# Performance work log

Measured on AMD Instinct MI355X. Metric: run time of the kernel, lower is better.

Reference implementation:

```python
import jax, jax.numpy as jnp
import numpy as np

BATCH, SEQ = 2, 4096
IN_FEATURES = 4096
OUT_FEATURES = 4096
BLOCK = 64                      # oft_block_size (bs)
RANK = IN_FEATURES // BLOCK     # number of diagonal blocks (r)


def setup_inputs() -> dict:
    key = jax.random.key(0)
    k1, k2, k3, k4 = jax.random.split(key, 4)
    x = jax.random.normal(k1, (BATCH, SEQ, IN_FEATURES), dtype=jnp.float32)
    # OFT adapter parameters: one (bs x bs) generator per block
    oft_r = jax.random.normal(k2, (RANK, BLOCK, BLOCK), dtype=jnp.float32) * 0.02
    # Dequantized GPTQ weight (out_features x in_features) + bias
    W = jax.random.normal(k3, (OUT_FEATURES, IN_FEATURES), dtype=jnp.float32) * 0.02
    b = jax.random.normal(k4, (OUT_FEATURES,), dtype=jnp.float32)
    return {"x": x, "oft_r": oft_r, "W": W, "b": b}


def _cayley_batch(data):
    # data: [r, bs, bs].  Q = (I - skew) @ (I + skew)^{-1}  (torch.linalg.solve left=False)
    bs = data.shape[-1]
    skew = 0.5 * (data - jnp.swapaxes(data, -1, -2))
    I = jnp.eye(bs, dtype=data.dtype)
    A = I + skew   # [r, bs, bs]
    B = I - skew
    # Solve Q A = B  ->  A^T Q^T = B^T
    Qt = jnp.linalg.solve(jnp.swapaxes(A, -1, -2), jnp.swapaxes(B, -1, -2))
    return jnp.swapaxes(Qt, -1, -2)


def reference(x, oft_r, W, b):
    rank, bs, _ = oft_r.shape
    # oft_rotation starts as identity; single active adapter -> rotation = Cayley(oft_r)
    oft_rotation = _cayley_batch(oft_r)            # [rank, bs, bs]
    batch_dims = x.shape[:-1]
    x_reshaped = x.reshape(*batch_dims, rank, bs)  # [..., r, k]
    x_rot = jnp.einsum('...rk,rkc->...rc', x_reshaped, oft_rotation)
    x_rot = x_rot.reshape(*batch_dims, rank * bs)  # [..., in_features]
    # quant_linear_module (dequantized): y = x_rot @ W^T + b
    return jnp.einsum('bsi,oi->bso', x_rot, W) + b
```

## Files before the change

### kernel.cpp

```cpp
#include <hip/hip_runtime.h>
#include <hip/hip_bf16.h>
#include <stdint.h>


typedef __bf16 bf16;
typedef __attribute__((ext_vector_type(4))) __bf16 bf16x4;
typedef __attribute__((ext_vector_type(8))) __bf16 bf16x8;
typedef __attribute__((ext_vector_type(4))) float f32x4;

__device__ __forceinline__ bf16 f2bf(float f) {
  unsigned u = __builtin_bit_cast(unsigned, f);
  u += 0x7fffu + ((u >> 16) & 1u);
  unsigned short h = (unsigned short)(u >> 16);
  return __builtin_bit_cast(bf16, h);
}

__global__ __launch_bounds__(256) void prep_kernel(const float* __restrict__ oft_r,
                                                   float* __restrict__ Qxt,
                                                   const float* __restrict__ x,
                                                   bf16* __restrict__ xb, long n) {
  __shared__ float St[64][68];
  __shared__ float Ta[64][65];
  __shared__ float Tb[64][65];
  const int tid = threadIdx.x;

  if (blockIdx.x >= 64) {
    long i0 = ((long)(blockIdx.x - 64) * 256 + tid) * 8;
    long stride = (long)(gridDim.x - 64) * 256 * 8;
    for (long i = i0; i < n; i += stride) {
      f32x4 a = *reinterpret_cast<const f32x4*>(x + i);
      f32x4 b = *reinterpret_cast<const f32x4*>(x + i + 4);
      bf16x8 o;
      o[0] = f2bf(a[0]); o[1] = f2bf(a[1]); o[2] = f2bf(a[2]); o[3] = f2bf(a[3]);
      o[4] = f2bf(b[0]); o[5] = f2bf(b[1]); o[6] = f2bf(b[2]); o[7] = f2bf(b[3]);
      *reinterpret_cast<bf16x8*>(xb + i) = o;
    }
    return;
  }

  const int r = blockIdx.x;
  const float* D = oft_r + (size_t)r * 4096;

  for (int idx = tid; idx < 4096; idx += 256) {
    int i = idx >> 6, j = idx & 63;
    float s = 0.5f * (D[i * 64 + j] - D[j * 64 + i]);
    St[j][i] = s;
    Ta[i][j] = (i == j ? 1.0f : 0.0f) - s;
  }
  __syncthreads();

  const int j = tid & 63;
  const int w = tid >> 6;
  float (*Tin)[65] = Ta;
  float (*Tout)[65] = Tb;

  for (int it = 0; it < 5; ++it) {
    float out[16];
#pragma unroll
    for (int m = 0; m < 16; ++m) out[m] = ((w * 16 + m) == j ? 1.0f : 0.0f);
    for (int c = 0; c < 64; ++c) {
      float tc = Tin[c][j];
      f32x4 s0 = *reinterpret_cast<const f32x4*>(&St[c][w * 16]);
      f32x4 s1 = *reinterpret_cast<const f32x4*>(&St[c][w * 16 + 4]);
      f32x4 s2 = *reinterpret_cast<const f32x4*>(&St[c][w * 16 + 8]);
      f32x4 s3 = *reinterpret_cast<const f32x4*>(&St[c][w * 16 + 12]);
#pragma unroll
      for (int q = 0; q < 4; ++q) {
        out[q]      -= s0[q] * tc;
        out[4 + q]  -= s1[q] * tc;
        out[8 + q]  -= s2[q] * tc;
        out[12 + q] -= s3[q] * tc;
      }
    }
#pragma unroll
    for (int m = 0; m < 16; ++m) Tout[w * 16 + m][j] = out[m];
    __syncthreads();
    float (*tmp)[65] = Tin; Tin = Tout; Tout = tmp;
  }
  {
    float out[16];
#pragma unroll
    for (int m = 0; m < 16; ++m) out[m] = Tin[w * 16 + m][j];
    for (int c = 0; c < 64; ++c) {
      float tc = Tin[c][j];
      f32x4 s0 = *reinterpret_cast<const f32x4*>(&St[c][w * 16]);
      f32x4 s1 = *reinterpret_cast<const f32x4*>(&St[c][w * 16 + 4]);
      f32x4 s2 = *reinterpret_cast<const f32x4*>(&St[c][w * 16 + 8]);
      f32x4 s3 = *reinterpret_cast<const f32x4*>(&St[c][w * 16 + 12]);
#pragma unroll
      for (int q = 0; q < 4; ++q) {
        out[q]      -= s0[q] * tc;
        out[4 + q]  -= s1[q] * tc;
        out[8 + q]  -= s2[q] * tc;
        out[12 + q] -= s3[q] * tc;
      }
    }
#pragma unroll
    for (int m = 0; m < 16; ++m) Qxt[(size_t)r * 4096 + (w * 16 + m) * 64 + j] = out[m];
  }
}

__global__ __launch_bounds__(256) void fold_w_kernel(const float* __restrict__ W,
                                                     const float* __restrict__ Qxt,
                                                     bf16* __restrict__ Wp) {
  __shared__ bf16 Wb[128 * 64];
  __shared__ bf16 Xt[64 * 64];
  const int tid = threadIdx.x;
  const int lane = tid & 63;
  const int wave = tid >> 6;
  const int o0 = blockIdx.x * 128;
  const int r = blockIdx.y;
  const int fr = lane & 15;
  const int kg = lane >> 4;

#pragma unroll
  for (int i = 0; i < 8; ++i) {
    int c = i * 256 + tid;
    int row = c >> 4, c4 = c & 15;
    f32x4 v = *reinterpret_cast<const f32x4*>(W + (size_t)(o0 + row) * 4096 + r * 64 + c4 * 4);
    bf16x4 o; o[0] = f2bf(v[0]); o[1] = f2bf(v[1]); o[2] = f2bf(v[2]); o[3] = f2bf(v[3]);
    *reinterpret_cast<bf16x4*>(&Wb[row * 64 + c4 * 4]) = o;
  }
#pragma unroll
  for (int i = 0; i < 4; ++i) {
    int c = i * 256 + tid;
    int row = c >> 4, c4 = c & 15;
    f32x4 v = *reinterpret_cast<const f32x4*>(Qxt + (size_t)r * 4096 + row * 64 + c4 * 4);
    bf16x4 o; o[0] = f2bf(v[0]); o[1] = f2bf(v[1]); o[2] = f2bf(v[2]); o[3] = f2bf(v[3]);
    *reinterpret_cast<bf16x4*>(&Xt[row * 64 + c4 * 4]) = o;
  }
  __syncthreads();

  const int wm = wave * 32;
  f32x4 acc[2][4];
#pragma unroll
  for (int mi = 0; mi < 2; ++mi)
#pragma unroll
    for (int ni = 0; ni < 4; ++ni) acc[mi][ni] = (f32x4){0.f, 0.f, 0.f, 0.f};

#pragma unroll
  for (int kk = 0; kk < 64; kk += 32) {
    bf16x8 af[2], bx[4];
#pragma unroll
    for (int mi = 0; mi < 2; ++mi)
      af[mi] = *reinterpret_cast<const bf16x8*>(&Wb[(wm + mi * 16 + fr) * 64 + kk + kg * 8]);
#pragma unroll
    for (int ni = 0; ni < 4; ++ni)
      bx[ni] = *reinterpret_cast<const bf16x8*>(&Xt[(ni * 16 + fr) * 64 + kk + kg * 8]);
#pragma unroll
    for (int mi = 0; mi < 2; ++mi)
#pragma unroll
      for (int ni = 0; ni < 4; ++ni)
        acc[mi][ni] = __builtin_amdgcn_mfma_f32_16x16x32_bf16(af[mi], bx[ni], acc[mi][ni], 0, 0, 0);
  }

#pragma unroll
  for (int mi = 0; mi < 2; ++mi)
#pragma unroll
    for (int ni = 0; ni < 4; ++ni)
#pragma unroll
      for (int q = 0; q < 4; ++q) {
        int row = o0 + wm + mi * 16 + kg * 4 + q;
        int col = ni * 16 + fr;
        Wp[(size_t)row * 4096 + r * 64 + col] = f2bf(acc[mi][ni][q]);
      }
}


#define GLDS16(g, l) __builtin_amdgcn_global_load_lds( \
    (const __attribute__((address_space(1))) unsigned int*)(g), \
    (__attribute__((address_space(3))) unsigned int*)(l), 16, 0, 0)

#define VMCNT4 asm volatile("s_waitcnt vmcnt(4)" ::: "memory")
#define VMCNT0 asm volatile("s_waitcnt vmcnt(0)" ::: "memory")
#define BARRIER() do { asm volatile("" ::: "memory"); \
  __builtin_amdgcn_s_barrier(); asm volatile("" ::: "memory"); } while (0)

#define MFMA16(AF, BF, RB) \
  _Pragma("unroll") \
  for (int m_ = 0; m_ < 4; ++m_) \
    _Pragma("unroll") \
    for (int n_ = 0; n_ < 4; ++n_) \
      acc[RB + m_][n_] = __builtin_amdgcn_mfma_f32_16x16x32_bf16(AF[m_], BF[n_], acc[RB + m_][n_], 0, 0, 0);

#define DO_TILE(BUF, TN, PRE) do { \
     \
    _Pragma("unroll") for (int n_ = 0; n_ < 4; ++n_) Ob[n_] = LDB(BUF, 0, n_); \
    _Pragma("unroll") for (int m_ = 0; m_ < 4; ++m_) Oa[m_] = LDA(BUF, 0, m_); \
    if (PRE) STAGE(TN, BUF ^ 1, 0); \
    BARRIER(); \
    __builtin_amdgcn_s_setprio(1); MFMA16(Oa, Ob, 0) __builtin_amdgcn_s_setprio(0); \
    BARRIER(); \
     \
    _Pragma("unroll") for (int m_ = 0; m_ < 4; ++m_) Ea[m_] = LDA(BUF, 0, 4 + m_); \
    if (PRE) STAGE(TN, BUF ^ 1, 1); \
    if (PRE) { VMCNT4; } else { VMCNT0; } \
    BARRIER(); \
    __builtin_amdgcn_s_setprio(1); MFMA16(Ea, Ob, 4) __builtin_amdgcn_s_setprio(0); \
    BARRIER(); \
     \
    _Pragma("unroll") for (int n_ = 0; n_ < 4; ++n_) Eb[n_] = LDB(BUF, 1, n_); \
    _Pragma("unroll") for (int m_ = 0; m_ < 4; ++m_) Oa[m_] = LDA(BUF, 1, m_); \
    if (PRE) STAGE(TN, BUF ^ 1, 2); \
    BARRIER(); \
    __builtin_amdgcn_s_setprio(1); MFMA16(Oa, Eb, 0) __builtin_amdgcn_s_setprio(0); \
    BARRIER(); \
     \
    _Pragma("unroll") for (int m_ = 0; m_ < 4; ++m_) Ea[m_] = LDA(BUF, 1, 4 + m_); \
    if (PRE) STAGE(TN, BUF ^ 1, 3); \
    if (PRE) { VMCNT4; } else { VMCNT0; } \
    BARRIER(); \
    __builtin_amdgcn_s_setprio(1); MFMA16(Ea, Eb, 4) __builtin_amdgcn_s_setprio(0); \
    BARRIER(); \
  } while (0)

__global__ __launch_bounds__(512, 2) void gemm_kernel(const bf16* __restrict__ A,
                                                      const bf16* __restrict__ B,
                                                      const float* __restrict__ bias,
                                                      float* __restrict__ C,
                                                      int M, int N, int K) {
  __shared__ bf16 lds[65536];
  const int tid = threadIdx.x;
  const int lane = tid & 63;
  const int wave = tid >> 6;
  const int wr = wave >> 2;
  const int wc = wave & 3;
  const int fr = lane & 15;
  const int kg = lane >> 4;
  const int m0 = blockIdx.y * 256;
  const int n0 = blockIdx.x * 256;
  const int NT = K >> 6;

  f32x4 acc[8][4];
#pragma unroll
  for (int m = 0; m < 8; ++m)
#pragma unroll
    for (int n = 0; n < 4; ++n) acc[m][n] = (f32x4){0.f, 0.f, 0.f, 0.f};

  auto STAGE = [&](int t, int db, int p) {
    const int op = p & 1, ks = p >> 1;
    const bf16* src = op ? B : A;
    const int base_row = op ? n0 : m0;
    const int ldsb = db * 32768 + op * 16384 + ks * 8192;
#pragma unroll
    for (int i = 0; i < 2; ++i) {
      int c = i * 512 + tid;
      int row = c >> 2, cc = c & 3;
      const bf16* g = src + (size_t)(base_row + row) * K + t * 64 + ks * 32
                      + ((cc ^ ((row >> 1) & 3)) << 3);
      GLDS16(g, &lds[ldsb + ((i * 512 + wave * 64) << 3)]);
    }
  };
  auto LDA = [&](int buf, int ks, int mi) -> bf16x8 {
    int row = wr * 128 + mi * 16 + fr;
    return *reinterpret_cast<const bf16x8*>(
        &lds[buf * 32768 + ks * 8192 + row * 32 + ((kg ^ ((row >> 1) & 3)) << 3)]);
  };
  auto LDB = [&](int buf, int ks, int ni) -> bf16x8 {
    int row = wc * 64 + ni * 16 + fr;
    return *reinterpret_cast<const bf16x8*>(
        &lds[buf * 32768 + 16384 + ks * 8192 + row * 32 + ((kg ^ ((row >> 1) & 3)) << 3)]);
  };

#pragma unroll
  for (int p = 0; p < 4; ++p) STAGE(0, 0, p);
  VMCNT4;
  BARRIER();

  bf16x8 Oa[4], Ob[4], Ea[4], Eb[4];
  for (int t = 0; t < NT; t += 2) {
    DO_TILE(0, t + 1, true);
    DO_TILE(1, t + 2, (t + 2) < NT);
  }

#pragma unroll
  for (int n = 0; n < 4; ++n) {
    int col = n0 + wc * 64 + n * 16 + fr;
    float bv = bias[col];
#pragma unroll
    for (int m = 0; m < 8; ++m) {
      int row0 = m0 + wr * 128 + m * 16 + kg * 4;
#pragma unroll
      for (int q = 0; q < 4; ++q)
        C[(size_t)(row0 + q) * N + col] = acc[m][n][q] + bv;
    }
  }
}

extern "C" void kernel_launch(void* const* d_in, const int* in_sizes, int n_in,
                              void* d_out, int out_size, void* d_ws, size_t ws_size,
                              hipStream_t stream) {
  const float* x     = (const float*)d_in[0];
  const float* oft_r = (const float*)d_in[1];
  const float* W     = (const float*)d_in[2];
  const float* b     = (const float*)d_in[3];
  float* y = (float*)d_out;

  char* ws = (char*)d_ws;
  float* Qxt = (float*)ws;
  bf16*  Wp  = (bf16*)(ws + (1u << 20));
  bf16*  xb  = (bf16*)(ws + (1u << 20) + (32u << 20));

  prep_kernel<<<2112, 256, 0, stream>>>(oft_r, Qxt, x, xb, 33554432L);
  dim3 fg(32, 64);
  fold_w_kernel<<<fg, 256, 0, stream>>>(W, Qxt, Wp);
  dim3 gg(4096 / 256, 8192 / 256);
  gemm_kernel<<<gg, 512, 0, stream>>>(xb, Wp, b, y, 8192, 4096, 4096);
}
```

Baseline: 316.3 us.

## Use five-slot LDS ring to prefetch GEMM tiles two steps ahead

The GEMM main loop moves from a double-buffered 64-wide K tile to a five-slot ring of 32-wide K half-tiles in LDS. Global loads are issued about two tiles ahead, with wait counts set to vmcnt(12) so more loads stay in flight, and the tail is drained explicitly. This is meant to hide more global-load latency behind the MFMA work. LDS per block grows to 160 KB and the loop count is hardcoded for K=4096.

Result: faster. 310.0 us (-2.0%).

```diff
diff --git a/kernel.cpp b/kernel.cpp
--- a/kernel.cpp
+++ b/kernel.cpp
@@ -171,8 +171,10 @@
     (const __attribute__((address_space(1))) unsigned int*)(g), \
     (__attribute__((address_space(3))) unsigned int*)(l), 16, 0, 0)
 
-#define VMCNT4 asm volatile("s_waitcnt vmcnt(4)" ::: "memory")
-#define VMCNT0 asm volatile("s_waitcnt vmcnt(0)" ::: "memory")
+#define VMCNT12 asm volatile("s_waitcnt vmcnt(12)" ::: "memory")
+#define VMCNT8  asm volatile("s_waitcnt vmcnt(8)" ::: "memory")
+#define VMCNT4  asm volatile("s_waitcnt vmcnt(4)" ::: "memory")
+#define VMCNT0  asm volatile("s_waitcnt vmcnt(0)" ::: "memory")
 #define BARRIER() do { asm volatile("" ::: "memory"); \
   __builtin_amdgcn_s_barrier(); asm volatile("" ::: "memory"); } while (0)
 
@@ -183,32 +185,32 @@
     for (int n_ = 0; n_ < 4; ++n_) \
       acc[RB + m_][n_] = __builtin_amdgcn_mfma_f32_16x16x32_bf16(AF[m_], BF[n_], acc[RB + m_][n_], 0, 0, 0);
 
-#define DO_TILE(BUF, TN, PRE) do { \
+#define DO_T(S0, S1, SA, SB, TN, PRE, W2, W1) do { \
      \
-    _Pragma("unroll") for (int n_ = 0; n_ < 4; ++n_) Ob[n_] = LDB(BUF, 0, n_); \
-    _Pragma("unroll") for (int m_ = 0; m_ < 4; ++m_) Oa[m_] = LDA(BUF, 0, m_); \
-    if (PRE) STAGE(TN, BUF ^ 1, 0); \
+    _Pragma("unroll") for (int n_ = 0; n_ < 4; ++n_) Ob[n_] = LDB(S0, n_); \
+    _Pragma("unroll") for (int m_ = 0; m_ < 4; ++m_) Oa[m_] = LDA(S0, m_); \
+    if (PRE) STG_A(TN, SA, 0); \
     BARRIER(); \
     __builtin_amdgcn_s_setprio(1); MFMA16(Oa, Ob, 0) __builtin_amdgcn_s_setprio(0); \
     BARRIER(); \
      \
-    _Pragma("unroll") for (int m_ = 0; m_ < 4; ++m_) Ea[m_] = LDA(BUF, 0, 4 + m_); \
-    if (PRE) STAGE(TN, BUF ^ 1, 1); \
-    if (PRE) { VMCNT4; } else { VMCNT0; } \
+    _Pragma("unroll") for (int m_ = 0; m_ < 4; ++m_) Ea[m_] = LDA(S0, 4 + m_); \
+    if (PRE) STG_B(TN, SA, 0); \
+    W2; \
     BARRIER(); \
     __builtin_amdgcn_s_setprio(1); MFMA16(Ea, Ob, 4) __builtin_amdgcn_s_setprio(0); \
     BARRIER(); \
      \
-    _Pragma("unroll") for (int n_ = 0; n_ < 4; ++n_) Eb[n_] = LDB(BUF, 1, n_); \
-    _Pragma("unroll") for (int m_ = 0; m_ < 4; ++m_) Oa[m_] = LDA(BUF, 1, m_); \
-    if (PRE) STAGE(TN, BUF ^ 1, 2); \
+    _Pragma("unroll") for (int n_ = 0; n_ < 4; ++n_) Eb[n_] = LDB(S1, n_); \
+    _Pragma("unroll") for (int m_ = 0; m_ < 4; ++m_) Oa[m_] = LDA(S1, m_); \
+    if (PRE) STG_A(TN, SB, 1); \
     BARRIER(); \
     __builtin_amdgcn_s_setprio(1); MFMA16(Oa, Eb, 0) __builtin_amdgcn_s_setprio(0); \
     BARRIER(); \
      \
-    _Pragma("unroll") for (int m_ = 0; m_ < 4; ++m_) Ea[m_] = LDA(BUF, 1, 4 + m_); \
-    if (PRE) STAGE(TN, BUF ^ 1, 3); \
-    if (PRE) { VMCNT4; } else { VMCNT0; } \
+    _Pragma("unroll") for (int m_ = 0; m_ < 4; ++m_) Ea[m_] = LDA(S1, 4 + m_); \
+    if (PRE) STG_B(TN, SB, 1); \
+    W1; \
     BARRIER(); \
     __builtin_amdgcn_s_setprio(1); MFMA16(Ea, Eb, 4) __builtin_amdgcn_s_setprio(0); \
     BARRIER(); \
@@ -219,7 +221,7 @@
                                                       const float* __restrict__ bias,
                                                       float* __restrict__ C,
                                                       int M, int N, int K) {
-  __shared__ bf16 lds[65536];
+  __shared__ bf16 lds[81920];
   const int tid = threadIdx.x;
   const int lane = tid & 63;
   const int wave = tid >> 6;
@@ -229,7 +231,6 @@
   const int kg = lane >> 4;
   const int m0 = blockIdx.y * 256;
   const int n0 = blockIdx.x * 256;
-  const int NT = K >> 6;
 
   f32x4 acc[8][4];
 #pragma unroll
@@ -237,41 +238,47 @@
 #pragma unroll
     for (int n = 0; n < 4; ++n) acc[m][n] = (f32x4){0.f, 0.f, 0.f, 0.f};
 
-  auto STAGE = [&](int t, int db, int p) {
-    const int op = p & 1, ks = p >> 1;
-    const bf16* src = op ? B : A;
-    const int base_row = op ? n0 : m0;
-    const int ldsb = db * 32768 + op * 16384 + ks * 8192;
+  auto STG = [&](const bf16* src, int base_row, int t, int ks, int ldsbase) {
 #pragma unroll
     for (int i = 0; i < 2; ++i) {
       int c = i * 512 + tid;
       int row = c >> 2, cc = c & 3;
       const bf16* g = src + (size_t)(base_row + row) * K + t * 64 + ks * 32
                       + ((cc ^ ((row >> 1) & 3)) << 3);
-      GLDS16(g, &lds[ldsb + ((i * 512 + wave * 64) << 3)]);
+      GLDS16(g, &lds[ldsbase + ((i * 512 + wave * 64) << 3)]);
     }
   };
-  auto LDA = [&](int buf, int ks, int mi) -> bf16x8 {
+  auto STG_A = [&](int t, int slot, int ks) { STG(A, m0, t, ks, slot * 16384); };
+  auto STG_B = [&](int t, int slot, int ks) { STG(B, n0, t, ks, slot * 16384 + 8192); };
+
+  auto LDA = [&](int slot, int mi) -> bf16x8 {
     int row = wr * 128 + mi * 16 + fr;
     return *reinterpret_cast<const bf16x8*>(
-        &lds[buf * 32768 + ks * 8192 + row * 32 + ((kg ^ ((row >> 1) & 3)) << 3)]);
+        &lds[slot * 16384 + row * 32 + ((kg ^ ((row >> 1) & 3)) << 3)]);
   };
-  auto LDB = [&](int buf, int ks, int ni) -> bf16x8 {
+  auto LDB = [&](int slot, int ni) -> bf16x8 {
     int row = wc * 64 + ni * 16 + fr;
     return *reinterpret_cast<const bf16x8*>(
-        &lds[buf * 32768 + 16384 + ks * 8192 + row * 32 + ((kg ^ ((row >> 1) & 3)) << 3)]);
+        &lds[slot * 16384 + 8192 + row * 32 + ((kg ^ ((row >> 1) & 3)) << 3)]);
   };
 
-#pragma unroll
-  for (int p = 0; p < 4; ++p) STAGE(0, 0, p);
-  VMCNT4;
+  STG_A(0, 0, 0); STG_B(0, 0, 0); STG_A(0, 1, 1); STG_B(0, 1, 1);
+  STG_A(1, 2, 0); STG_B(1, 2, 0); STG_A(1, 3, 1); STG_B(1, 3, 1);
+  VMCNT12;
   BARRIER();
 
   bf16x8 Oa[4], Ob[4], Ea[4], Eb[4];
-  for (int t = 0; t < NT; t += 2) {
-    DO_TILE(0, t + 1, true);
-    DO_TILE(1, t + 2, (t + 2) < NT);
-  }
+  for (int t = 0; t < 60; t += 5) {
+    DO_T(0, 1, 4, 0, t + 2, true, VMCNT12, VMCNT12);
+    DO_T(2, 3, 1, 2, t + 3, true, VMCNT12, VMCNT12);
+    DO_T(4, 0, 3, 4, t + 4, true, VMCNT12, VMCNT12);
+    DO_T(1, 2, 0, 1, t + 5, true, VMCNT12, VMCNT12);
+    DO_T(3, 4, 2, 3, t + 6, true, VMCNT12, VMCNT12);
+  }
+  DO_T(0, 1, 4, 0, 62, true,  VMCNT12, VMCNT12);
+  DO_T(2, 3, 1, 2, 63, true,  VMCNT12, VMCNT12);
+  DO_T(4, 0, 0, 0, 0,  false, VMCNT8,  VMCNT4);
+  DO_T(1, 2, 0, 0, 0,  false, VMCNT0,  VMCNT0);
 
 #pragma unroll
   for (int n = 0; n < 4; ++n) {
@@ -303,7 +310,7 @@
 
   prep_kernel<<<2112, 256, 0, stream>>>(oft_r, Qxt, x, xb, 33554432L);
   dim3 fg(32, 64);
-  fold_w_kernel<<<fg, 256, 0, stream>>>(W, Qxt, Wp);
+  fold_w_kernel<<<fg, 64 * 4, 0, stream>>>(W, Qxt, Wp);
   dim3 gg(4096 / 256, 8192 / 256);
   gemm_kernel<<<gg, 512, 0, stream>>>(xb, Wp, b, y, 8192, 4096, 4096);
 }
```
